# Performance work log

Measured on AMD Instinct MI355X. Metric: run time of the kernel, lower is better.

## Reference

```python
import jax, jax.numpy as jnp
import numpy as np

EPS = 1e-9


def setup_inputs() -> dict:
    key = jax.random.key(0)
    kE, kQ, kK, kV = jax.random.split(key, 4)
    B, S, D = 8, 2048, 256
    return {
        "E": jax.random.normal(kE, (B, S, D), dtype=jnp.float32),
        "WQ": jax.random.normal(kQ, (D, D), dtype=jnp.float32) * (1.0 / np.sqrt(D)),
        "WK": jax.random.normal(kK, (D, D), dtype=jnp.float32) * (1.0 / np.sqrt(D)),
        "WV": jax.random.normal(kV, (D, D), dtype=jnp.float32) * (1.0 / np.sqrt(D)),
    }


def reference(E, WQ, WK, WV):
    # E: [B, S, D]; WQ/WK/WV: [D, D] (torch Linear weight, applied as x @ W.T)
    D = E.shape[-1]
    scale = jnp.asarray(np.sqrt(D), dtype=E.dtype)
    Q = jnp.einsum('bsd,ed->bse', E, WQ)
    K = jnp.einsum('bsd,ed->bse', E, WK)
    V = jnp.einsum('bsd,ed->bse', E, WV)
    # Full score matrix [B, S, S] (non-flash, as in the original)
    W = jnp.einsum('bqd,bkd->bqk', Q, K) / scale
    # mask=True path: causal tril mask, additionally zeroed where W == 0 exactly
    S_len = W.shape[-1]
    tril = jnp.tril(jnp.ones((S_len, S_len), dtype=W.dtype))  # [S, S]
    M = jnp.where(W == 0, jnp.zeros_like(W), tril[None, :, :])
    # custom masked softmax with epsilon denominator
    x_max = jnp.max(W, axis=-1, keepdims=True)
    x_exp = jnp.exp(W - x_max) * M
    A = x_exp / (jnp.sum(x_exp, axis=-1, keepdims=True) + EPS)
    return jnp.einsum('bqk,bkd->bqd', A, V)
```

## Files before the change

### kernel.cpp

```cpp
#include <hip/hip_runtime.h>
#include <stdint.h>


typedef __attribute__((ext_vector_type(8)))  short bf16x8;
typedef __attribute__((ext_vector_type(4)))  float f32x4;
typedef __attribute__((ext_vector_type(16))) float f32x16;

#define NEGF -3.0e38f
#define LDP  40

__device__ __forceinline__ unsigned short f2bf(float f){
  union { float f; unsigned u; } v; v.f = f;
  unsigned r = v.u + 0x7FFFu + ((v.u >> 16) & 1u);
  return (unsigned short)(r >> 16);
}
__device__ __forceinline__ unsigned pk2(float a, float b){
  return (unsigned)f2bf(a) | ((unsigned)f2bf(b) << 16);
}

__global__ void wconv_kernel(const float* __restrict__ WQ, const float* __restrict__ WK,
                             const float* __restrict__ WV, unsigned short* __restrict__ Wb)
{
  const int widx = blockIdx.x, kk = blockIdx.y, n = threadIdx.x;
  const float* W = (widx==0) ? WQ : ((widx==1) ? WK : WV);
  unsigned short* dst = Wb + (size_t)widx*65536 + kk*8192 + n*32;
#pragma unroll
  for (int gp=0; gp<4; ++gp){
    const int g = gp ^ (n & 3);
    const float* src = W + (size_t)n*256 + kk*32 + g*8;
    float4 a = *reinterpret_cast<const float4*>(src);
    float4 c = *reinterpret_cast<const float4*>(src + 4);
    uint4 v; v.x = pk2(a.x,a.y); v.y = pk2(a.z,a.w); v.z = pk2(c.x,c.y); v.w = pk2(c.z,c.w);
    *reinterpret_cast<uint4*>(dst + gp*8) = v;
  }
}

__global__ __launch_bounds__(256) void qkv_proj_kernel(
    const float* __restrict__ E, const unsigned short* __restrict__ Wb,
    unsigned short* __restrict__ Qb, unsigned short* __restrict__ Ka,
    unsigned short* __restrict__ Vf)
{
  __shared__ unsigned short As[32*256];
  __shared__ unsigned short Bs[2][8192];

  const int m0 = blockIdx.x * 32;
  const int b  = m0 >> 11;
  const int sb = m0 & 2047;
  const int t = threadIdx.x, lane = t & 63, w = t >> 6;
  const int hi = lane >> 4, lo = lane & 15;

  auto stageB = [&](int widx, int kk, int buf){
    const char* src = (const char*)Wb + widx*131072 + kk*16384;
    char* dst = (char*)Bs[buf];
#pragma unroll
    for (int c=0;c<4;c++){
      const int off = c*4096 + t*16;
      __builtin_amdgcn_global_load_lds(
        (const __attribute__((address_space(1))) unsigned int*)(src + off),
        (__attribute__((address_space(3))) unsigned int*)(dst + off), 16, 0, 0);
    }
  };

  stageB(0, 0, 0);
  {
    const int r = t >> 3, c0 = (t & 7) * 32;
    const float* ga = E + (size_t)(m0 + r)*256 + c0;
#pragma unroll
    for (int gg=0; gg<4; ++gg){
      float4 x = *reinterpret_cast<const float4*>(ga + gg*8);
      float4 y = *reinterpret_cast<const float4*>(ga + gg*8 + 4);
      uint4 v; v.x = pk2(x.x,x.y); v.y = pk2(x.z,x.w); v.z = pk2(y.x,y.y); v.w = pk2(y.z,y.w);
      const int g = (t & 7)*4 + gg;
      *reinterpret_cast<uint4*>((char*)As + r*512 + ((g ^ (r & 7)) << 4)) = v;
    }
  }
  __syncthreads();

  const f32x4 fzero = {0.f,0.f,0.f,0.f};
  const int u = sb >> 5;
  for (int widx=0; widx<3; ++widx){
    f32x4 acc[2][4];
#pragma unroll
    for (int mi=0;mi<2;mi++)
#pragma unroll
      for (int f=0;f<4;f++) acc[mi][f] = fzero;
    if (widx) stageB(widx, 0, 0);

    for (int kk=0; kk<8; ++kk){
      const int bb = kk & 1;
      asm volatile("s_waitcnt vmcnt(0)" ::: "memory");
      __syncthreads();
      if (kk < 7) stageB(widx, kk+1, bb^1);

      bf16x8 afr[2], bfr[4];
#pragma unroll
      for (int mi=0;mi<2;mi++){
        const int r = mi*16 + lo;
        afr[mi] = *reinterpret_cast<const bf16x8*>(
            (const char*)As + r*512 + (((kk*4 + hi) ^ (r & 7)) << 4));
      }
#pragma unroll
      for (int f=0;f<4;f++){
        const int n = w*64 + f*16 + lo;
        bfr[f] = *reinterpret_cast<const bf16x8*>(
            (const char*)Bs[bb] + n*64 + ((hi ^ (n & 3)) << 4));
      }
#pragma unroll
      for (int mi=0;mi<2;mi++)
#pragma unroll
        for (int f=0;f<4;f++)
          acc[mi][f] = __builtin_amdgcn_mfma_f32_16x16x32_bf16(afr[mi], bfr[f], acc[mi][f], 0,0,0);
    }

    if (widx == 0){
#pragma unroll
      for (int mi=0;mi<2;mi++)
#pragma unroll
        for (int f=0;f<4;f++){
          const int col = w*64 + f*16 + lo;
#pragma unroll
          for (int r=0;r<4;r++)
            Qb[(size_t)(m0 + mi*16 + hi*4 + r)*256 + col] = f2bf(acc[mi][f][r]*0.0625f);
        }
    } else if (widx == 1){
      unsigned short* Kab = Ka + (size_t)b*524288 + (size_t)u*8192;
#pragma unroll
      for (int mi=0;mi<2;mi++)
#pragma unroll
        for (int f=0;f<4;f++){
          const int c = w*4 + f;
          const int j = lo & 7;
          const int lb = 32*(lo>>3) + mi*16 + hi*4;
#pragma unroll
          for (int r=0;r<4;r++)
            Kab[(size_t)(c*64 + lb + r)*8 + j] = f2bf(acc[mi][f][r]);
        }
    } else {
      unsigned short* Vfb = Vf + (size_t)b*524288;
#pragma unroll
      for (int mi=0;mi<2;mi++)
#pragma unroll
        for (int f=0;f<4;f++){
          const int d  = w*64 + f*16 + lo;
          const int dt = d >> 5;
          const int l  = 32*(hi&1) + (d&31);
          const int j0 = 4*(hi>>1);
          unsigned short* vp = Vfb + ((size_t)((u*2 + mi)*8 + dt)*64 + l)*8 + j0;
          uint2 pw; pw.x = pk2(acc[mi][f][0], acc[mi][f][1]);
          pw.y = pk2(acc[mi][f][2], acc[mi][f][3]);
          *reinterpret_cast<uint2*>(vp) = pw;
        }
    }
  }
}

__global__ __launch_bounds__(256, 2) void attn_kernel(
    const unsigned short* __restrict__ Qb, const unsigned short* __restrict__ Ka,
    const unsigned short* __restrict__ Vf, float* __restrict__ Out,
    const int split, float* __restrict__ P1, float* __restrict__ ML)
{
  __shared__ char Kt[2][16384];

  const int bid  = blockIdx.x;
  const int b    = bid & 7;
  const int cidx = bid >> 3;
  int tau, chunk, mode, u0, u1;
  if (split){
    if (cidx < 32){
      tau = 31 - (cidx >> 1); chunk = cidx & 1;
      u0 = chunk ? (tau + 1) : 0;
      u1 = chunk ? (2*tau + 2) : (tau + 1);
      mode = 1 + chunk;
    } else { tau = 47 - cidx; chunk = 0; u0 = 0; u1 = 2*tau + 2; mode = 0; }
  } else { tau = 31 - cidx; chunk = 0; u0 = 0; u1 = 2*tau + 2; mode = 0; }
  const int Qbase = tau * 64;

  const int t = threadIdx.x;
  const int lane = t & 63, w = t >> 6;
  const int qs = w >> 1, dh = w & 1;
  const int l31 = lane & 31, h5 = lane >> 5;
  const int q_l = Qbase + qs*32 + l31;
  const int diagu = 2*tau + qs;

  const char* Kab = (const char*)Ka + (size_t)b*1048576;
  const char* Vfb = (const char*)Vf + (size_t)b*1048576;

  auto stage = [&](int uu){
    const char* src = Kab + (size_t)uu*16384;
    char* dstl = (char*)Kt[uu & 1];
#pragma unroll
    for (int i=0;i<4;i++){
      const int off = i*4096 + t*16;
      __builtin_amdgcn_global_load_lds(
        (const __attribute__((address_space(1))) unsigned int*)(src + off),
        (__attribute__((address_space(3))) unsigned int*)(dstl + off), 16, 0, 0);
    }
  };

  bf16x8 qf[16];
  {
    const unsigned short* Qp = Qb + ((size_t)(b*2048 + q_l))*256 + h5*8;
#pragma unroll
    for (int c=0;c<16;c++) qf[c] = *reinterpret_cast<const bf16x8*>(Qp + c*16);
  }

  const f32x16 z16 = {0.f,0.f,0.f,0.f,0.f,0.f,0.f,0.f,0.f,0.f,0.f,0.f,0.f,0.f,0.f,0.f};
  f32x16 accO[4];
#pragma unroll
  for (int i=0;i<4;i++) accO[i] = z16;
  float m_run = NEGF, l_run = 0.f;

  stage(u0);

  for (int u = u0; u < u1; ++u){
    asm volatile("s_waitcnt vmcnt(0)" ::: "memory");
    __builtin_amdgcn_s_barrier();
    if (u + 1 < u1) stage(u+1);

    const char* Vu = Vfb + (size_t)u*16384 + dh*4096 + lane*16;
    bf16x8 vf0[4], vf1[4];
#pragma unroll
    for (int i=0;i<4;i++){
      vf0[i] = *reinterpret_cast<const bf16x8*>(Vu + i*1024);
      vf1[i] = *reinterpret_cast<const bf16x8*>(Vu + 8192 + i*1024);
    }

    const char* kt = Kt[u & 1];
    f32x16 sv0 = z16, sv1 = z16;
#pragma unroll
    for (int c=0;c<16;c+=2){
      bf16x8 a0 = *reinterpret_cast<const bf16x8*>(kt + c*1024 + lane*16);
      bf16x8 a1 = *reinterpret_cast<const bf16x8*>(kt + (c+1)*1024 + lane*16);
      sv0 = __builtin_amdgcn_mfma_f32_32x32x16_bf16(a0, qf[c],   sv0, 0,0,0);
      sv1 = __builtin_amdgcn_mfma_f32_32x32x16_bf16(a1, qf[c+1], sv1, 0,0,0);
    }
    f32x16 s16 = sv0 + sv1;

    if (u >= diagu){
      const int kvb = u*32 + 4*h5;
#pragma unroll
      for (int r=0;r<16;r++){
        const int kv = kvb + (r&3) + 8*(r>>2);
        if (kv > q_l) s16[r] = NEGF;
      }
    }

    float t8[8], t4[4];
#pragma unroll
    for (int i=0;i<8;i++) t8[i] = fmaxf(s16[i], s16[i+8]);
#pragma unroll
    for (int i=0;i<4;i++) t4[i] = fmaxf(t8[i], t8[i+4]);
    float pmax = fmaxf(fmaxf(t4[0],t4[1]), fmaxf(t4[2],t4[3]));
    pmax = fmaxf(pmax, __shfl_xor(pmax, 32, 64));

    if (!__all(pmax - m_run <= 8.0f)){
      const float mn = fmaxf(m_run, pmax);
      const float alpha = __expf(m_run - mn);
#pragma unroll
      for (int i=0;i<4;i++) accO[i] *= alpha;
      l_run *= alpha;
      m_run = mn;
    }
    float p[16];
#pragma unroll
    for (int r=0;r<16;r++) p[r] = __expf(s16[r] - m_run);
#pragma unroll
    for (int i=0;i<8;i++) t8[i] = p[i] + p[i+8];
#pragma unroll
    for (int i=0;i<4;i++) t4[i] = t8[i] + t8[i+4];
    float ls = (t4[0]+t4[1]) + (t4[2]+t4[3]);
    ls += __shfl_xor(ls, 32, 64);
    l_run += ls;

    union { bf16x8 v; unsigned u32[4]; } pa0, pa1;
#pragma unroll
    for (int k=0;k<4;k++){
      pa0.u32[k] = pk2(p[2*k],   p[2*k+1]);
      pa1.u32[k] = pk2(p[8+2*k], p[9+2*k]);
    }

#pragma unroll
    for (int i=0;i<4;i++){
      accO[i] = __builtin_amdgcn_mfma_f32_32x32x16_bf16(vf0[i], pa0.v, accO[i], 0,0,0);
      accO[i] = __builtin_amdgcn_mfma_f32_32x32x16_bf16(vf1[i], pa1.v, accO[i], 0,0,0);
    }
  }

  if (mode && dh == 0 && lane < 32){
    float* mlp = ML + ((size_t)((b*16 + (tau-16))*2 + chunk)*64 + qs*32 + lane)*2;
    mlp[0] = m_run; mlp[1] = l_run;
  }

  __syncthreads();

  const float inv = (mode == 0) ? 1.0f/(l_run + 1e-9f) : 1.0f;
  float* Tw = (float*)(&Kt[0][0]) + w*2048;
  const int qloc = lane >> 1, dc = (lane & 1) * 16;
#pragma unroll
  for (int i=0;i<4;i++){
#pragma unroll
    for (int r=0;r<16;r++)
      Tw[l31*33 + ((r&3) + 8*(r>>2) + 4*h5)] = accO[i][r] * inv;
    asm volatile("s_waitcnt lgkmcnt(0)" ::: "memory");
    __builtin_amdgcn_sched_barrier(0);
    float* dst = (mode <= 1)
      ? (Out + ((size_t)(b*2048 + Qbase + qs*32 + qloc))*256 + dh*128 + i*32 + dc)
      : (P1 + ((size_t)((b*16 + (tau-16))*64 + qs*32 + qloc))*256 + dh*128 + i*32 + dc);
#pragma unroll
    for (int k=0;k<4;k++){
      float4 vv = { Tw[qloc*33 + dc + 4*k],     Tw[qloc*33 + dc + 4*k + 1],
                    Tw[qloc*33 + dc + 4*k + 2], Tw[qloc*33 + dc + 4*k + 3] };
      *reinterpret_cast<float4*>(dst + 4*k) = vv;
    }
    asm volatile("s_waitcnt lgkmcnt(0)" ::: "memory");
    __builtin_amdgcn_sched_barrier(0);
  }
}

__global__ void combine_kernel(float* __restrict__ Out, const float* __restrict__ P1,
                               const float* __restrict__ ML)
{
  const int bid = blockIdx.x;
  const int b = bid >> 4, tt = bid & 15;
  const int t = threadIdx.x;
  const int q = t >> 2, dg = (t & 3) * 64;
  const size_t mlb = ((size_t)(b*16 + tt)*2)*64 + q;
  const float m0 = ML[mlb*2],          l0 = ML[mlb*2 + 1];
  const float m1 = ML[(mlb + 64)*2],   l1 = ML[(mlb + 64)*2 + 1];
  const float M = fmaxf(m0, m1);
  const float e0 = __expf(m0 - M), e1 = __expf(m1 - M);
  const float inv = 1.0f/(e0*l0 + e1*l1 + 1e-9f);
  float* O = Out + ((size_t)(b*2048 + (16 + tt)*64 + q))*256 + dg;
  const float* P = P1 + ((size_t)((b*16 + tt)*64 + q))*256 + dg;
#pragma unroll
  for (int k=0;k<16;k++){
    float4 a = *reinterpret_cast<const float4*>(O + k*4);
    float4 c = *reinterpret_cast<const float4*>(P + k*4);
    float4 o;
    o.x = (e0*a.x + e1*c.x)*inv; o.y = (e0*a.y + e1*c.y)*inv;
    o.z = (e0*a.z + e1*c.z)*inv; o.w = (e0*a.w + e1*c.w)*inv;
    *reinterpret_cast<float4*>(O + k*4) = o;
  }
}

extern "C" void kernel_launch(void* const* d_in, const int* in_sizes, int n_in,
                              void* d_out, int out_size, void* d_ws, size_t ws_size,
                              hipStream_t stream)
{
  const float* E  = (const float*)d_in[0];
  const float* WQ = (const float*)d_in[1];
  const float* WK = (const float*)d_in[2];
  const float* WV = (const float*)d_in[3];
  const size_t elems = (size_t)8*2048*256;

  unsigned short* Qb = (unsigned short*)d_ws;
  unsigned short* Ka = Qb + elems;
  unsigned short* Vf = Ka + elems;
  unsigned short* Wb = Vf + elems;
  float* P1 = (float*)((char*)d_ws + 3*elems*2 + 393216);
  float* ML = P1 + (size_t)8*16*64*256;

  const size_t NEED_MIN  = 3*elems*2 + 393216;
  const size_t NEED_FULL = NEED_MIN + ((size_t)8*16*64*256 + 32768)*4;
  if (ws_size < NEED_MIN) return;
  const int split = (ws_size >= NEED_FULL) ? 1 : 0;

  wconv_kernel<<<dim3(3,8), 256, 0, stream>>>(WQ, WK, WV, Wb);
  qkv_proj_kernel<<<512, 256, 0, stream>>>(E, Wb, Qb, Ka, Vf);
  attn_kernel<<<split ? 384 : 256, 256, 0, stream>>>(Qb, Ka, Vf, (float*)d_out, split, P1, ML);
  if (split) combine_kernel<<<128, 256, 0, stream>>>((float*)d_out, P1, ML);
}
```

Before: 101.3 us.

## Split attention KV range into fixed 8-tile chunks with bf16 partials and multi-way combine

```diff
diff --git a/kernel.cpp b/kernel.cpp
--- a/kernel.cpp
+++ b/kernel.cpp
@@ -6,8 +6,8 @@
 typedef __attribute__((ext_vector_type(4)))  float f32x4;
 typedef __attribute__((ext_vector_type(16))) float f32x16;
 
-#define NEGF -3.0e38f
-#define LDP  40
+#define NEGF  -3.0e38f
+#define MINIT -1.0e30f
 
 __device__ __forceinline__ unsigned short f2bf(float f){
   union { float f; unsigned u; } v; v.f = f;
@@ -16,6 +16,9 @@
 }
 __device__ __forceinline__ unsigned pk2(float a, float b){
   return (unsigned)f2bf(a) | ((unsigned)f2bf(b) << 16);
+}
+__device__ __forceinline__ float bf2f(unsigned short h){
+  union { unsigned u; float f; } v; v.u = ((unsigned)h) << 16; return v.f;
 }
 
 __global__ void wconv_kernel(const float* __restrict__ WQ, const float* __restrict__ WK,
@@ -154,25 +157,35 @@
   }
 }
 
-__global__ __launch_bounds__(256, 2) void attn_kernel(
+__global__ __launch_bounds__(256, 4) void attn_kernel(
     const unsigned short* __restrict__ Qb, const unsigned short* __restrict__ Ka,
     const unsigned short* __restrict__ Vf, float* __restrict__ Out,
-    const int split, float* __restrict__ P1, float* __restrict__ ML)
+    const int sched, unsigned short* __restrict__ Pb, float* __restrict__ ML,
+    const int psl, const int mls)
 {
   __shared__ char Kt[2][16384];
 
   const int bid  = blockIdx.x;
   const int b    = bid & 7;
   const int cidx = bid >> 3;
-  int tau, chunk, mode, u0, u1;
-  if (split){
-    if (cidx < 32){
-      tau = 31 - (cidx >> 1); chunk = cidx & 1;
-      u0 = chunk ? (tau + 1) : 0;
-      u1 = chunk ? (2*tau + 2) : (tau + 1);
-      mode = 1 + chunk;
-    } else { tau = 47 - cidx; chunk = 0; u0 = 0; u1 = 2*tau + 2; mode = 0; }
-  } else { tau = 31 - cidx; chunk = 0; u0 = 0; u1 = 2*tau + 2; mode = 0; }
+
+  int tau = cidx, chunk = 0, pbase = 0, mlbase = 0, nch = 1;
+  if (sched){
+    int rem = cidx;
+    for (tau = 0;; ++tau){
+      nch = (sched == 2) ? ((tau >> 2) + 1) : ((tau >> 4) + 1);
+      if (rem < nch) break;
+      rem -= nch;
+      pbase  += nch - 1;
+      mlbase += (nch > 1) ? nch : 0;
+    }
+    chunk = rem;
+  }
+  int u0, u1;
+  if (sched == 2){ u0 = chunk*8; u1 = min(u0 + 8, 2*tau + 2); }
+  else if (sched == 1){ u0 = chunk*(tau+1); u1 = chunk ? (2*tau+2) : (tau+1); }
+  else { u0 = 0; u1 = 2*tau + 2; }
+  const int mode = (nch == 1) ? 0 : (chunk == 0 ? 1 : 2);
   const int Qbase = tau * 64;
 
   const int t = threadIdx.x;
@@ -208,7 +221,7 @@
   f32x16 accO[4];
 #pragma unroll
   for (int i=0;i<4;i++) accO[i] = z16;
-  float m_run = NEGF, l_run = 0.f;
+  float m_run = MINIT, l_run = 0.f;
 
   stage(u0);
 
@@ -287,7 +300,7 @@
   }
 
   if (mode && dh == 0 && lane < 32){
-    float* mlp = ML + ((size_t)((b*16 + (tau-16))*2 + chunk)*64 + qs*32 + lane)*2;
+    float* mlp = ML + ((size_t)(b*mls + mlbase + chunk)*64 + qs*32 + lane)*2;
     mlp[0] = m_run; mlp[1] = l_run;
   }
 
@@ -303,43 +316,89 @@
       Tw[l31*33 + ((r&3) + 8*(r>>2) + 4*h5)] = accO[i][r] * inv;
     asm volatile("s_waitcnt lgkmcnt(0)" ::: "memory");
     __builtin_amdgcn_sched_barrier(0);
-    float* dst = (mode <= 1)
-      ? (Out + ((size_t)(b*2048 + Qbase + qs*32 + qloc))*256 + dh*128 + i*32 + dc)
-      : (P1 + ((size_t)((b*16 + (tau-16))*64 + qs*32 + qloc))*256 + dh*128 + i*32 + dc);
-#pragma unroll
-    for (int k=0;k<4;k++){
-      float4 vv = { Tw[qloc*33 + dc + 4*k],     Tw[qloc*33 + dc + 4*k + 1],
-                    Tw[qloc*33 + dc + 4*k + 2], Tw[qloc*33 + dc + 4*k + 3] };
-      *reinterpret_cast<float4*>(dst + 4*k) = vv;
+    const float* srcT = &Tw[qloc*33 + dc];
+    if (mode < 2){
+      float* dst = Out + ((size_t)(b*2048 + Qbase + qs*32 + qloc))*256 + dh*128 + i*32 + dc;
+#pragma unroll
+      for (int k=0;k<4;k++){
+        float4 vv = { srcT[4*k], srcT[4*k+1], srcT[4*k+2], srcT[4*k+3] };
+        *reinterpret_cast<float4*>(dst + 4*k) = vv;
+      }
+    } else {
+      unsigned short* pb = Pb + ((size_t)(b*psl + pbase + chunk-1)*64 + qs*32 + qloc)*256
+                              + dh*128 + i*32 + dc;
+      uint4 w0, w1;
+      w0.x = pk2(srcT[0],  srcT[1]);  w0.y = pk2(srcT[2],  srcT[3]);
+      w0.z = pk2(srcT[4],  srcT[5]);  w0.w = pk2(srcT[6],  srcT[7]);
+      w1.x = pk2(srcT[8],  srcT[9]);  w1.y = pk2(srcT[10], srcT[11]);
+      w1.z = pk2(srcT[12], srcT[13]); w1.w = pk2(srcT[14], srcT[15]);
+      *reinterpret_cast<uint4*>(pb)     = w0;
+      *reinterpret_cast<uint4*>(pb + 8) = w1;
     }
     asm volatile("s_waitcnt lgkmcnt(0)" ::: "memory");
     __builtin_amdgcn_sched_barrier(0);
   }
 }
 
-__global__ void combine_kernel(float* __restrict__ Out, const float* __restrict__ P1,
-                               const float* __restrict__ ML)
+__global__ void combine_kernel(float* __restrict__ Out, const unsigned short* __restrict__ Pb,
+                               const float* __restrict__ ML, const int sched,
+                               const int psl, const int mls)
 {
-  const int bid = blockIdx.x;
-  const int b = bid >> 4, tt = bid & 15;
+  const int b = blockIdx.x & 7, tidx = blockIdx.x >> 3;
+  const int tau = tidx + ((sched == 2) ? 4 : 16);
+  int pbase = 0, mlbase = 0;
+  for (int j = 0; j < tau; ++j){
+    const int nj = (sched == 2) ? ((j >> 2) + 1) : ((j >> 4) + 1);
+    pbase  += nj - 1;
+    mlbase += (nj > 1) ? nj : 0;
+  }
+  const int nch = (sched == 2) ? ((tau >> 2) + 1) : ((tau >> 4) + 1);
+
   const int t = threadIdx.x;
   const int q = t >> 2, dg = (t & 3) * 64;
-  const size_t mlb = ((size_t)(b*16 + tt)*2)*64 + q;
-  const float m0 = ML[mlb*2],          l0 = ML[mlb*2 + 1];
-  const float m1 = ML[(mlb + 64)*2],   l1 = ML[(mlb + 64)*2 + 1];
-  const float M = fmaxf(m0, m1);
-  const float e0 = __expf(m0 - M), e1 = __expf(m1 - M);
-  const float inv = 1.0f/(e0*l0 + e1*l1 + 1e-9f);
-  float* O = Out + ((size_t)(b*2048 + (16 + tt)*64 + q))*256 + dg;
-  const float* P = P1 + ((size_t)((b*16 + tt)*64 + q))*256 + dg;
+
+  float mc[8], lc[8];
+#pragma unroll
+  for (int c=0;c<8;c++){
+    if (c < nch){
+      const float* mlp = ML + ((size_t)(b*mls + mlbase + c)*64 + q)*2;
+      mc[c] = mlp[0]; lc[c] = mlp[1];
+    } else { mc[c] = NEGF; lc[c] = 0.f; }
+  }
+  float M = mc[0];
+#pragma unroll
+  for (int c=1;c<8;c++) M = fmaxf(M, mc[c]);
+  float e[8], L = 0.f;
+#pragma unroll
+  for (int c=0;c<8;c++){ e[c] = __expf(mc[c] - M); L += e[c]*lc[c]; }
+  const float inv = 1.0f/(L + 1e-9f);
+
+  float* O = Out + ((size_t)(b*2048 + tau*64 + q))*256 + dg;
+  f32x4 acc[16];
 #pragma unroll
   for (int k=0;k<16;k++){
-    float4 a = *reinterpret_cast<const float4*>(O + k*4);
-    float4 c = *reinterpret_cast<const float4*>(P + k*4);
-    float4 o;
-    o.x = (e0*a.x + e1*c.x)*inv; o.y = (e0*a.y + e1*c.y)*inv;
-    o.z = (e0*a.z + e1*c.z)*inv; o.w = (e0*a.w + e1*c.w)*inv;
-    *reinterpret_cast<float4*>(O + k*4) = o;
+    float4 v = *reinterpret_cast<const float4*>(O + 4*k);
+    acc[k][0] = e[0]*v.x; acc[k][1] = e[0]*v.y; acc[k][2] = e[0]*v.z; acc[k][3] = e[0]*v.w;
+  }
+#pragma unroll
+  for (int c=1;c<8;c++){
+    if (c < nch){
+      const unsigned short* pr = Pb + ((size_t)(b*psl + pbase + c-1)*64 + q)*256 + dg;
+#pragma unroll
+      for (int k=0;k<8;k++){
+        uint4 pv = *reinterpret_cast<const uint4*>(pr + 8*k);
+        const unsigned short* us = (const unsigned short*)&pv;
+#pragma unroll
+        for (int j=0;j<4;j++) acc[2*k][j]   += e[c]*bf2f(us[j]);
+#pragma unroll
+        for (int j=0;j<4;j++) acc[2*k+1][j] += e[c]*bf2f(us[4+j]);
+      }
+    }
+  }
+#pragma unroll
+  for (int k=0;k<16;k++){
+    float4 v = { acc[k][0]*inv, acc[k][1]*inv, acc[k][2]*inv, acc[k][3]*inv };
+    *reinterpret_cast<float4*>(O + 4*k) = v;
   }
 }
 
@@ -357,16 +416,24 @@
   unsigned short* Ka = Qb + elems;
   unsigned short* Vf = Ka + elems;
   unsigned short* Wb = Vf + elems;
-  float* P1 = (float*)((char*)d_ws + 3*elems*2 + 393216);
-  float* ML = P1 + (size_t)8*16*64*256;
-
-  const size_t NEED_MIN  = 3*elems*2 + 393216;
-  const size_t NEED_FULL = NEED_MIN + ((size_t)8*16*64*256 + 32768)*4;
-  if (ws_size < NEED_MIN) return;
-  const int split = (ws_size >= NEED_FULL) ? 1 : 0;
+  const size_t base = 3*elems*2 + 393216;
+
+  const size_t PB_F = (size_t)8*112*64*256*2, ML_F = (size_t)8*140*64*2*4;
+  const size_t PB_C = (size_t)8*16*64*256*2,  ML_C = (size_t)8*32*64*2*4;
+  const size_t NEED_FINE   = base + PB_F + ML_F;
+  const size_t NEED_COARSE = base + PB_C + ML_C;
+  if (ws_size < base) return;
+  const int sched = (ws_size >= NEED_FINE) ? 2 : (ws_size >= NEED_COARSE) ? 1 : 0;
+  const int psl = (sched == 2) ? 112 : 16;
+  const int mls = (sched == 2) ? 140 : 32;
+  unsigned short* Pb = (unsigned short*)((char*)d_ws + base);
+  float* ML = (float*)((char*)d_ws + base + ((sched == 2) ? PB_F : PB_C));
 
   wconv_kernel<<<dim3(3,8), 256, 0, stream>>>(WQ, WK, WV, Wb);
   qkv_proj_kernel<<<512, 256, 0, stream>>>(E, Wb, Qb, Ka, Vf);
-  attn_kernel<<<split ? 384 : 256, 256, 0, stream>>>(Qb, Ka, Vf, (float*)d_out, split, P1, ML);
-  if (split) combine_kernel<<<128, 256, 0, stream>>>((float*)d_out, P1, ML);
-}
+  const int agrid = (sched == 2) ? 1152 : (sched == 1) ? 384 : 256;
+  attn_kernel<<<agrid, 256, 0, stream>>>(Qb, Ka, Vf, (float*)d_out, sched, Pb, ML, psl, mls);
+  if (sched)
+    combine_kernel<<<(sched == 2) ? 224 : 128, 256, 0, stream>>>(
+        (float*)d_out, Pb, ML, sched, psl, mls);
+}
```

Result: slower. 180.2 us (+77.9%).
